# Kernel tuning notes

Measured on AMD Instinct MI355X. Metric: run time of the kernel, lower is better.

The kernel has to match this reference:

```python
import jax, jax.numpy as jnp
import numpy as np

C, H, W, D, M = 64, 512, 512, 4, 16


def setup_inputs() -> dict:
    key = jax.random.key(0)
    ks = jax.random.split(key, 9)
    scale = (1.0 / (C * C)) ** 0.5
    return {
        "q": jax.random.normal(ks[0], (1, 1, H, W), jnp.float32),
        "proj_w": jax.random.normal(ks[1], (C, 1, 1, 1), jnp.float32),
        "proj_b": jax.random.normal(ks[2], (C, 1, 1), jnp.float32) * 0.01,
        "spec_wr": jax.random.normal(ks[3], (D, C, C, M, M), jnp.float32) * scale,
        "spec_wi": jax.random.normal(ks[4], (D, C, C, M, M), jnp.float32) * scale,
        "w_w": jax.random.normal(ks[5], (D, C, C, 1, 1), jnp.float32) * (1.0 / C ** 0.5),
        "w_b": jax.random.normal(ks[6], (D, C, 1, 1), jnp.float32) * 0.01,
        "final_w": jax.random.normal(ks[7], (1, C, 1, 1), jnp.float32) * (1.0 / C ** 0.5),
        "final_b": jax.random.normal(ks[8], (1, 1, 1), jnp.float32) * 0.01,
    }


def _spectral(x, wr, wi, m):
    # x: (C,H,W). FFT2 -> contract low modes -> zero-pad -> iFFT2, take real part.
    Cin, Hh, Ww = x.shape
    x_ft = jnp.fft.fft2(x, axes=(-2, -1))  # (C,H,W) complex
    w = (wr + 1j * wi).astype(x_ft.dtype)  # (Cin,Cout,m,m)
    out_sub = jnp.einsum('imn,iomn->omn', x_ft[:, :m, :m], w)
    out_ft = jnp.zeros((wr.shape[1], Hh, Ww), dtype=x_ft.dtype).at[:, :m, :m].set(out_sub)
    return jnp.fft.ifft2(out_ft, axes=(-2, -1)).real


def reference(q, proj_w, proj_b, spec_wr, spec_wi, w_w, w_b, final_w, final_b):
    m = spec_wr.shape[-1]
    depth = spec_wr.shape[0]
    x = q[0].astype(jnp.float32)  # (C_in,H,W) -- batch must be 1
    # 1x1 conv lift
    x = jnp.einsum('oi,ihw->ohw', proj_w[:, :, 0, 0], x) + proj_b
    for d in range(depth):
        x_spec = _spectral(x, spec_wr[d], spec_wi[d], m)
        x_local = jnp.einsum('oi,ihw->ohw', w_w[d, :, :, 0, 0], x) + w_b[d]
        x = jax.nn.gelu(x_spec + x_local)
    x = jnp.einsum('oi,ihw->ohw', final_w[:, :, 0, 0], x) + final_b
    return x[None]  # re-add batch dim
```

## Files before the change

kernel.cpp:

```cpp
#include <hip/hip_runtime.h>
#include <cmath>

#define CC 64
#define HH 512
#define WWID 512
#define HWSZ (HH*WWID)
#define DEPTH 4

typedef __attribute__((ext_vector_type(8))) short short8;
typedef __attribute__((ext_vector_type(4))) float floatx4;

__device__ inline unsigned short f2bf(float f){
  unsigned int u = __float_as_uint(f);
  u += 0x7FFF + ((u >> 16) & 1);
  return (unsigned short)(u >> 16);
}
__device__ inline float bf2f(unsigned short h){
  return __uint_as_float(((unsigned int)h) << 16);
}

__global__ void k_init(const float* __restrict__ ww,
                       float* __restrict__ ctab, float* __restrict__ stab,
                       unsigned short* __restrict__ trigBh, unsigned short* __restrict__ trigBl,
                       unsigned short* __restrict__ trigTh, unsigned short* __restrict__ trigTl,
                       unsigned short* __restrict__ Whi, unsigned short* __restrict__ Wlo,
                       float4* __restrict__ Xfz){
  if (blockIdx.x < 32) Xfz[blockIdx.x*256 + threadIdx.x] = make_float4(0.f,0.f,0.f,0.f);
  int idx = blockIdx.x*256 + threadIdx.x;
  if (idx < 8192){
    int pos = idx >> 4, k = idx & 15;
    int r = (pos * k) & 511;
    double ang = (2.0 * 3.14159265358979323846 / 512.0) * (double)r;
    float c = (float)cos(ang), s = (float)sin(ang);
    ctab[idx] = c;  stab[idx] = s;
    unsigned short ch = f2bf(c), sh = f2bf(s);
    unsigned short cl = f2bf(c - bf2f(ch)), sl = f2bf(s - bf2f(sh));
    trigBh[pos*32 + 2*k]     = ch;  trigBl[pos*32 + 2*k]     = cl;
    trigBh[pos*32 + 2*k + 1] = sh;  trigBl[pos*32 + 2*k + 1] = sl;
    trigTh[(2*k)*512 + pos]   = ch;  trigTl[(2*k)*512 + pos]   = cl;
    trigTh[(2*k+1)*512 + pos] = sh;  trigTl[(2*k+1)*512 + pos] = sl;
  } else {
    int t = idx - 8192;
    float v = ww[t];
    unsigned short h = f2bf(v);
    Whi[t] = h;  Wlo[t] = f2bf(v - bf2f(h));
  }
}

#define APITCH 136
#define XPITCH 33
template<int LIFT>
__global__ __launch_bounds__(256) void k_dftw(const unsigned int* __restrict__ xp,
    const float* __restrict__ qsrc, const float* __restrict__ pw, const float* __restrict__ pb,
    const unsigned short* __restrict__ trigTh, const unsigned short* __restrict__ trigTl,
    const float* __restrict__ ctab, const float* __restrict__ stab,
    float* __restrict__ Xfa, float4* __restrict__ Yz){
  if (blockIdx.x < 32) Yz[blockIdx.x*256 + threadIdx.x] = make_float4(0.f,0.f,0.f,0.f);

  __shared__ unsigned short Ahs[64*APITCH], Als[64*APITCH];
  __shared__ unsigned short Bhs[32*APITCH], Bls[32*APITCH];
  __shared__ float X1s[64*XPITCH];
  int row0 = blockIdx.x * 64;
  int i  = row0 >> 9;
  int h0 = row0 & 511;
  int t = threadIdx.x;
  int g = t >> 6, lm = t & 15, lq = (t >> 4) & 3;
  float pa = 0.f, pbv = 0.f;
  if (LIFT){ pa = pw[i]; pbv = pb[i]; }

  floatx4 acc[2] = {{0.f,0.f,0.f,0.f},{0.f,0.f,0.f,0.f}};

  for (int kc = 0; kc < 4; ++kc){
    {
      int r = t >> 2, qq = t & 3;
      unsigned int* dh = (unsigned int*)&Ahs[r*APITCH + qq*32];
      unsigned int* dl = (unsigned int*)&Als[r*APITCH + qq*32];
      if (LIFT){
        const float4* src4 = (const float4*)(qsrc + (size_t)(h0 + r)*512 + kc*128 + qq*32);
        #pragma unroll
        for (int u = 0; u < 8; ++u){
          float4 v = src4[u];
          v.x = fmaf(pa, v.x, pbv); v.y = fmaf(pa, v.y, pbv);
          v.z = fmaf(pa, v.z, pbv); v.w = fmaf(pa, v.w, pbv);
          unsigned short h0_ = f2bf(v.x), h1 = f2bf(v.y), h2 = f2bf(v.z), h3 = f2bf(v.w);
          unsigned short g0 = f2bf(v.x - bf2f(h0_)), g1 = f2bf(v.y - bf2f(h1));
          unsigned short g2 = f2bf(v.z - bf2f(h2)), g3 = f2bf(v.w - bf2f(h3));
          uint2 ph, pl;
          ph.x = (unsigned)h0_ | ((unsigned)h1 << 16);
          ph.y = (unsigned)h2 | ((unsigned)h3 << 16);
          pl.x = (unsigned)g0 | ((unsigned)g1 << 16);
          pl.y = (unsigned)g2 | ((unsigned)g3 << 16);
          *(uint2*)&dh[u*2] = ph;
          *(uint2*)&dl[u*2] = pl;
        }
      } else {
        const uint4* srcp = (const uint4*)(xp + ((size_t)(h0 + r)*64 + i)*512 + kc*128 + qq*32);
        #pragma unroll
        for (int u = 0; u < 8; ++u){
          uint4 v = srcp[u];
          uint2 ph, pl;
          ph.x = (v.x & 0xffffu) | (v.y << 16);
          ph.y = (v.z & 0xffffu) | (v.w << 16);
          pl.x = (v.x >> 16) | (v.y & 0xffff0000u);
          pl.y = (v.z >> 16) | (v.w & 0xffff0000u);
          *(uint2*)&dh[u*2] = ph;
          *(uint2*)&dl[u*2] = pl;
        }
      }
    }
    {
      int j = t >> 3, qq = t & 7;
      const uint4* sh = (const uint4*)((const unsigned int*)trigTh + j*256 + kc*64 + qq*8);
      const uint4* sl = (const uint4*)((const unsigned int*)trigTl + j*256 + kc*64 + qq*8);
      uint4* dh = (uint4*)&Bhs[j*APITCH + qq*16];
      uint4* dl = (uint4*)&Bls[j*APITCH + qq*16];
      dh[0] = sh[0]; dh[1] = sh[1];
      dl[0] = sl[0]; dl[1] = sl[1];
    }
    __syncthreads();
    #pragma unroll
    for (int ks = 0; ks < 4; ++ks){
      short8 ah = *(const short8*)&Ahs[(g*16 + lm)*APITCH + ks*32 + lq*8];
      short8 al = *(const short8*)&Als[(g*16 + lm)*APITCH + ks*32 + lq*8];
      #pragma unroll
      for (int nt = 0; nt < 2; ++nt){
        short8 bh = *(const short8*)&Bhs[(nt*16 + lm)*APITCH + ks*32 + lq*8];
        short8 bl = *(const short8*)&Bls[(nt*16 + lm)*APITCH + ks*32 + lq*8];
        acc[nt] = __builtin_amdgcn_mfma_f32_16x16x32_bf16(ah, bh, acc[nt], 0, 0, 0);
        acc[nt] = __builtin_amdgcn_mfma_f32_16x16x32_bf16(ah, bl, acc[nt], 0, 0, 0);
        acc[nt] = __builtin_amdgcn_mfma_f32_16x16x32_bf16(al, bh, acc[nt], 0, 0, 0);
      }
    }
    __syncthreads();
  }
  #pragma unroll
  for (int nt = 0; nt < 2; ++nt){
    int j = nt*16 + lm;
    float sgn = (j & 1) ? -1.f : 1.f;
    #pragma unroll
    for (int rg = 0; rg < 4; ++rg){
      int m = g*16 + lq*4 + rg;
      X1s[m*XPITCH + j] = sgn * acc[nt][rg];
    }
  }
  __syncthreads();

  int mo = t >> 4, n = t & 15;
  float ar = 0.f, ai = 0.f;
  #pragma unroll 8
  for (int hh = 0; hh < 64; ++hh){
    int h = h0 + hh;
    float Re = X1s[hh*XPITCH + 2*n];
    float Im = X1s[hh*XPITCH + 2*n + 1];
    float c = ctab[h*16 + mo], s = stab[h*16 + mo];
    ar += Re*c + Im*s;
    ai += Im*c - Re*s;
  }
  atomicAdd(&Xfa[(i*256 + t)*2],     ar);
  atomicAdd(&Xfa[(i*256 + t)*2 + 1], ai);
}

__global__ void k_contract(const float2* __restrict__ Xf,
                           const float* __restrict__ wr, const float* __restrict__ wi,
                           float* __restrict__ Ya){
  int o = blockIdx.x, ic = blockIdx.y;
  int mn = blockIdx.z*64 + threadIdx.x;
  float ar = 0.f, ai = 0.f;
  int i0 = ic * 16;
  #pragma unroll
  for (int ii = 0; ii < 16; ++ii){
    int i = i0 + ii;
    float2 xf = Xf[i*256 + mn];
    float wrv = wr[(i*64 + o)*256 + mn];
    float wiv = wi[(i*64 + o)*256 + mn];
    ar += xf.x*wrv - xf.y*wiv;
    ai += xf.x*wiv + xf.y*wrv;
  }
  const float sc = 1.f/262144.f;
  atomicAdd(&Ya[(o*256 + mn)*2],     ar*sc);
  atomicAdd(&Ya[(o*256 + mn)*2 + 1], ai*sc);
}

__global__ void k_idfth(const float2* __restrict__ Y, const float* __restrict__ ct,
                        const float* __restrict__ st,
                        unsigned int* __restrict__ Thi, unsigned int* __restrict__ Tlo,
                        float4* __restrict__ Xfz){
  if (blockIdx.x < 32) Xfz[blockIdx.x*256 + threadIdx.x] = make_float4(0.f,0.f,0.f,0.f);
  int idx = blockIdx.x*256 + threadIdx.x;
  int n = idx & 15, o = (idx >> 4) & 63, h = idx >> 10;
  float ar = 0.f, ai = 0.f;
  #pragma unroll
  for (int m = 0; m < 16; ++m){
    float2 y = Y[(o<<8) + (m<<4) + n];
    float c = ct[h*16 + m], s = st[h*16 + m];
    ar += y.x*c - y.y*s;
    ai += y.x*s + y.y*c;
  }
  float tr = ar, ts = -ai;
  unsigned short rh = f2bf(tr), sh = f2bf(ts);
  Thi[idx] = (unsigned int)rh | ((unsigned int)sh << 16);
  unsigned short rl = f2bf(tr - bf2f(rh)), slr = f2bf(ts - bf2f(sh));
  Tlo[idx] = (unsigned int)rl | ((unsigned int)slr << 16);
}

#define PITCH 104
template<int LIFT, int FINAL>
__global__ __launch_bounds__(256) void k_combine(
    const unsigned int* __restrict__ xp, const float* __restrict__ qsrc,
    const float* __restrict__ pw, const float* __restrict__ pb,
    const unsigned short* __restrict__ Whid, const unsigned short* __restrict__ Wlod,
    const unsigned int* __restrict__ Thi,  const unsigned int* __restrict__ Tlo,
    const unsigned short* __restrict__ trigBh, const unsigned short* __restrict__ trigBl,
    const float* __restrict__ wb, unsigned int* __restrict__ xo,
    const float* __restrict__ fw, const float* __restrict__ fb,
    float* __restrict__ outp)
{
  __shared__ unsigned short Ah[64*PITCH], Al[64*PITCH];
  int h  = blockIdx.y;
  int w0 = blockIdx.x * 128;
  int t  = threadIdx.x;

  {
    int o = t >> 2, q8 = t & 3;
    const uint4* sh = (const uint4*)((const unsigned int*)Whid + o*32 + q8*8);
    const uint4* sl = (const uint4*)((const unsigned int*)Wlod + o*32 + q8*8);
    uint4* dh = (uint4*)((unsigned int*)&Ah[o*PITCH] + q8*8);
    uint4* dl = (uint4*)((unsigned int*)&Al[o*PITCH] + q8*8);
    dh[0] = sh[0]; dh[1] = sh[1];
    dl[0] = sl[0]; dl[1] = sl[1];
  }
  {
    int o = t >> 2, q4 = t & 3;
    const uint4* sh = (const uint4*)(Thi + (size_t)h*1024 + o*16 + q4*4);
    const uint4* sl = (const uint4*)(Tlo + (size_t)h*1024 + o*16 + q4*4);
    uint4* dh = (uint4*)((unsigned int*)&Ah[o*PITCH + 64] + q4*4);
    uint4* dl = (uint4*)((unsigned int*)&Al[o*PITCH + 64] + q4*4);
    dh[0] = sh[0];
    dl[0] = sl[0];
  }
  __syncthreads();

  int g  = t >> 6;
  int lm = t & 15;
  int lq = (t >> 4) & 3;
  int wbase = w0 + g*32;

  const unsigned int* xw = xp + (size_t)h*32768;
  float pwv[16], pbv[16];
  if (LIFT){
    #pragma unroll
    for (int u = 0; u < 8; ++u){
      pwv[u]   = pw[lq*8 + u];      pbv[u]   = pb[lq*8 + u];
      pwv[8+u] = pw[32 + lq*8 + u]; pbv[8+u] = pb[32 + lq*8 + u];
    }
  }

  short8 bf0[2], bl0[2], bf1[2], bl1[2], bf2[2], bl2[2];
  #pragma unroll
  for (int nt = 0; nt < 2; ++nt){
    int w = wbase + nt*16 + lm;
    unsigned int v0[8], v1[8];
    if (LIFT){
      float qv = qsrc[(size_t)h*512 + w];
      #pragma unroll
      for (int u = 0; u < 8; ++u){
        float a = fmaf(pwv[u], qv, pbv[u]);
        unsigned short hh = f2bf(a), ll = f2bf(a - bf2f(hh));
        v0[u] = (unsigned int)hh | ((unsigned int)ll << 16);
        float b = fmaf(pwv[8+u], qv, pbv[8+u]);
        unsigned short hb = f2bf(b), lb = f2bf(b - bf2f(hb));
        v1[u] = (unsigned int)hb | ((unsigned int)lb << 16);
      }
    } else {
      #pragma unroll
      for (int u = 0; u < 8; ++u){
        v0[u] = xw[(size_t)(     lq*8 + u)*512 + w];
        v1[u] = xw[(size_t)(32 + lq*8 + u)*512 + w];
      }
    }
    unsigned int f0[4], l0[4], f1[4], l1[4];
    #pragma unroll
    for (int p = 0; p < 4; ++p){
      f0[p] = (v0[2*p] & 0xffffu) | (v0[2*p+1] << 16);
      l0[p] = (v0[2*p] >> 16)     | (v0[2*p+1] & 0xffff0000u);
      f1[p] = (v1[2*p] & 0xffffu) | (v1[2*p+1] << 16);
      l1[p] = (v1[2*p] >> 16)     | (v1[2*p+1] & 0xffff0000u);
    }
    bf0[nt] = *(short8*)f0;  bl0[nt] = *(short8*)l0;
    bf1[nt] = *(short8*)f1;  bl1[nt] = *(short8*)l1;
    bf2[nt] = *(const short8*)(trigBh + (size_t)w*32 + lq*8);
    bl2[nt] = *(const short8*)(trigBl + (size_t)w*32 + lq*8);
  }

  floatx4 acc[8] = {{0.f,0.f,0.f,0.f},{0.f,0.f,0.f,0.f},{0.f,0.f,0.f,0.f},{0.f,0.f,0.f,0.f},
                    {0.f,0.f,0.f,0.f},{0.f,0.f,0.f,0.f},{0.f,0.f,0.f,0.f},{0.f,0.f,0.f,0.f}};

  #pragma unroll
  for (int m = 0; m < 4; ++m){
    short8 af0 = *(const short8*)&Ah[(m*16 + lm)*PITCH +  0 + lq*8];
    short8 al0 = *(const short8*)&Al[(m*16 + lm)*PITCH +  0 + lq*8];
    short8 af1 = *(const short8*)&Ah[(m*16 + lm)*PITCH + 32 + lq*8];
    short8 al1 = *(const short8*)&Al[(m*16 + lm)*PITCH + 32 + lq*8];
    short8 af2 = *(const short8*)&Ah[(m*16 + lm)*PITCH + 64 + lq*8];
    short8 al2 = *(const short8*)&Al[(m*16 + lm)*PITCH + 64 + lq*8];
    #pragma unroll
    for (int nt = 0; nt < 2; ++nt){
      int a = m*2 + nt;
      acc[a] = __builtin_amdgcn_mfma_f32_16x16x32_bf16(af0, bf0[nt], acc[a], 0, 0, 0);
      acc[a] = __builtin_amdgcn_mfma_f32_16x16x32_bf16(af0, bl0[nt], acc[a], 0, 0, 0);
      acc[a] = __builtin_amdgcn_mfma_f32_16x16x32_bf16(al0, bf0[nt], acc[a], 0, 0, 0);
      acc[a] = __builtin_amdgcn_mfma_f32_16x16x32_bf16(af1, bf1[nt], acc[a], 0, 0, 0);
      acc[a] = __builtin_amdgcn_mfma_f32_16x16x32_bf16(af1, bl1[nt], acc[a], 0, 0, 0);
      acc[a] = __builtin_amdgcn_mfma_f32_16x16x32_bf16(al1, bf1[nt], acc[a], 0, 0, 0);
      acc[a] = __builtin_amdgcn_mfma_f32_16x16x32_bf16(af2, bf2[nt], acc[a], 0, 0, 0);
      acc[a] = __builtin_amdgcn_mfma_f32_16x16x32_bf16(af2, bl2[nt], acc[a], 0, 0, 0);
      acc[a] = __builtin_amdgcn_mfma_f32_16x16x32_bf16(al2, bf2[nt], acc[a], 0, 0, 0);
    }
  }

  if (!FINAL){
    #pragma unroll
    for (int m = 0; m < 4; ++m){
      #pragma unroll
      for (int nt = 0; nt < 2; ++nt){
        int w = wbase + nt*16 + lm;
        #pragma unroll
        for (int rg = 0; rg < 4; ++rg){
          int o = m*16 + lq*4 + rg;
          float u = acc[m*2+nt][rg] + wb[o];
          float z = 0.7978845608028654f * fmaf(0.044715f, u*u*u, u);
          float e = __expf(2.f*z);
          float gl = u - __fdividef(u, e + 1.f);
          unsigned short hi_ = f2bf(gl);
          unsigned short lo_ = f2bf(gl - bf2f(hi_));
          xo[((size_t)h*64 + o)*512 + w] = (unsigned int)hi_ | ((unsigned int)lo_ << 16);
        }
      }
    }
  } else {
    float* fred = (float*)Ah;
    __syncthreads();
    #pragma unroll
    for (int nt = 0; nt < 2; ++nt){
      float partial = 0.f;
      #pragma unroll
      for (int m = 0; m < 4; ++m){
        #pragma unroll
        for (int rg = 0; rg < 4; ++rg){
          int o = m*16 + lq*4 + rg;
          float u = acc[m*2+nt][rg] + wb[o];
          float z = 0.7978845608028654f * fmaf(0.044715f, u*u*u, u);
          float e = __expf(2.f*z);
          float gl = u - __fdividef(u, e + 1.f);
          partial = fmaf(fw[o], gl, partial);
        }
      }
      int wl = g*32 + nt*16 + lm;
      fred[wl*17 + lq] = partial;
    }
    __syncthreads();
    if (t < 128){
      float s = fb[0];
      #pragma unroll
      for (int k2 = 0; k2 < 4; ++k2) s += fred[t*17 + k2];
      outp[(size_t)h*512 + w0 + t] = s;
    }
  }
}

extern "C" void kernel_launch(void* const* d_in, const int* in_sizes, int n_in,
                              void* d_out, int out_size, void* d_ws, size_t ws_size,
                              hipStream_t stream) {
  const float* q       = (const float*)d_in[0];
  const float* proj_w  = (const float*)d_in[1];
  const float* proj_b  = (const float*)d_in[2];
  const float* spec_wr = (const float*)d_in[3];
  const float* spec_wi = (const float*)d_in[4];
  const float* w_w     = (const float*)d_in[5];
  const float* w_b     = (const float*)d_in[6];
  const float* final_w = (const float*)d_in[7];
  const float* final_b = (const float*)d_in[8];
  float* out = (float*)d_out;

  char* ws = (char*)d_ws;
  float*  ctab = (float*) (ws + 0);
  float*  stab = (float*) (ws + 32768);
  unsigned short* trigBh = (unsigned short*)(ws + 65536);
  unsigned short* trigBl = (unsigned short*)(ws + 98304);
  unsigned int* Thi = (unsigned int*)(ws + 131072);
  unsigned int* Tlo = (unsigned int*)(ws + 2228224);
  float*  Xf   = (float*) (ws + 4325376);
  float*  Y    = (float*) (ws + 4456448);
  unsigned int* x = (unsigned int*)(ws + 4587520);
  unsigned short* Whi = (unsigned short*)(ws + 71696384);
  unsigned short* Wlo = (unsigned short*)(ws + 71729152);
  unsigned short* trigTh = (unsigned short*)(ws + 71761920);
  unsigned short* trigTl = (unsigned short*)(ws + 71794688);

  k_init<<<96, 256, 0, stream>>>(w_w, ctab, stab, trigBh, trigBl, trigTh, trigTl,
                                 Whi, Wlo, (float4*)Xf);

  for (int d = 0; d < DEPTH; ++d){
    if (d == 0)
      k_dftw<1><<<512, 256, 0, stream>>>(x, q, proj_w, proj_b, trigTh, trigTl,
                                         ctab, stab, Xf, (float4*)Y);
    else
      k_dftw<0><<<512, 256, 0, stream>>>(x, q, proj_w, proj_b, trigTh, trigTl,
                                         ctab, stab, Xf, (float4*)Y);
    k_contract<<<dim3(64,4,4), 64, 0, stream>>>((const float2*)Xf,
                                                spec_wr + (size_t)d*1048576,
                                                spec_wi + (size_t)d*1048576, Y);
    k_idfth<<<2048, 256, 0, stream>>>((const float2*)Y, ctab, stab, Thi, Tlo,
                                      (float4*)Xf);
    if (d == 0)
      k_combine<1,0><<<dim3(4,512), 256, 0, stream>>>(x, q, proj_w, proj_b,
          Whi + d*4096, Wlo + d*4096, Thi, Tlo, trigBh, trigBl,
          w_b + d*64, x, final_w, final_b, out);
    else if (d < DEPTH-1)
      k_combine<0,0><<<dim3(4,512), 256, 0, stream>>>(x, q, proj_w, proj_b,
          Whi + d*4096, Wlo + d*4096, Thi, Tlo, trigBh, trigBl,
          w_b + d*64, x, final_w, final_b, out);
    else
      k_combine<0,1><<<dim3(4,512), 256, 0, stream>>>(x, q, proj_w, proj_b,
          Whi + d*4096, Wlo + d*4096, Thi, Tlo, trigBh, trigBl,
          w_b + d*64, x, final_w, final_b, out);
  }
}
```

Baseline: 327.9 us.

## Load DFT MFMA operands directly from global memory, dropping LDS staging

The W-direction DFT kernel no longer stages the activation rows and trig tables through shared memory with syncthreads per K chunk. Each lane now loads its MFMA A and B fragments straight from global memory (or q with the lift applied) and does the bf16 hi/lo split in registers. This removes the LDS round trip, the barriers and the shared-memory footprint, which may raise occupancy. In exchange, trig fragments are read redundantly per wave through the cache, and the global loads are less coalesced.

```diff
diff --git a/kernel.cpp b/kernel.cpp
--- a/kernel.cpp
+++ b/kernel.cpp
@@ -47,7 +47,6 @@
   }
 }
 
-#define APITCH 136
 #define XPITCH 33
 template<int LIFT>
 __global__ __launch_bounds__(256) void k_dftw(const unsigned int* __restrict__ xp,
@@ -57,8 +56,6 @@
     float* __restrict__ Xfa, float4* __restrict__ Yz){
   if (blockIdx.x < 32) Yz[blockIdx.x*256 + threadIdx.x] = make_float4(0.f,0.f,0.f,0.f);
 
-  __shared__ unsigned short Ahs[64*APITCH], Als[64*APITCH];
-  __shared__ unsigned short Bhs[32*APITCH], Bls[32*APITCH];
   __shared__ float X1s[64*XPITCH];
   int row0 = blockIdx.x * 64;
   int i  = row0 >> 9;
@@ -70,69 +67,52 @@
 
   floatx4 acc[2] = {{0.f,0.f,0.f,0.f},{0.f,0.f,0.f,0.f}};
 
-  for (int kc = 0; kc < 4; ++kc){
-    {
-      int r = t >> 2, qq = t & 3;
-      unsigned int* dh = (unsigned int*)&Ahs[r*APITCH + qq*32];
-      unsigned int* dl = (unsigned int*)&Als[r*APITCH + qq*32];
-      if (LIFT){
-        const float4* src4 = (const float4*)(qsrc + (size_t)(h0 + r)*512 + kc*128 + qq*32);
-        #pragma unroll
-        for (int u = 0; u < 8; ++u){
-          float4 v = src4[u];
-          v.x = fmaf(pa, v.x, pbv); v.y = fmaf(pa, v.y, pbv);
-          v.z = fmaf(pa, v.z, pbv); v.w = fmaf(pa, v.w, pbv);
-          unsigned short h0_ = f2bf(v.x), h1 = f2bf(v.y), h2 = f2bf(v.z), h3 = f2bf(v.w);
-          unsigned short g0 = f2bf(v.x - bf2f(h0_)), g1 = f2bf(v.y - bf2f(h1));
-          unsigned short g2 = f2bf(v.z - bf2f(h2)), g3 = f2bf(v.w - bf2f(h3));
-          uint2 ph, pl;
-          ph.x = (unsigned)h0_ | ((unsigned)h1 << 16);
-          ph.y = (unsigned)h2 | ((unsigned)h3 << 16);
-          pl.x = (unsigned)g0 | ((unsigned)g1 << 16);
-          pl.y = (unsigned)g2 | ((unsigned)g3 << 16);
-          *(uint2*)&dh[u*2] = ph;
-          *(uint2*)&dl[u*2] = pl;
-        }
-      } else {
-        const uint4* srcp = (const uint4*)(xp + ((size_t)(h0 + r)*64 + i)*512 + kc*128 + qq*32);
-        #pragma unroll
-        for (int u = 0; u < 8; ++u){
-          uint4 v = srcp[u];
-          uint2 ph, pl;
-          ph.x = (v.x & 0xffffu) | (v.y << 16);
-          ph.y = (v.z & 0xffffu) | (v.w << 16);
-          pl.x = (v.x >> 16) | (v.y & 0xffff0000u);
-          pl.y = (v.z >> 16) | (v.w & 0xffff0000u);
-          *(uint2*)&dh[u*2] = ph;
-          *(uint2*)&dl[u*2] = pl;
-        }
-      }
-    }
-    {
-      int j = t >> 3, qq = t & 7;
-      const uint4* sh = (const uint4*)((const unsigned int*)trigTh + j*256 + kc*64 + qq*8);
-      const uint4* sl = (const uint4*)((const unsigned int*)trigTl + j*256 + kc*64 + qq*8);
-      uint4* dh = (uint4*)&Bhs[j*APITCH + qq*16];
-      uint4* dl = (uint4*)&Bls[j*APITCH + qq*16];
-      dh[0] = sh[0]; dh[1] = sh[1];
-      dl[0] = sl[0]; dl[1] = sl[1];
-    }
-    __syncthreads();
-    #pragma unroll
-    for (int ks = 0; ks < 4; ++ks){
-      short8 ah = *(const short8*)&Ahs[(g*16 + lm)*APITCH + ks*32 + lq*8];
-      short8 al = *(const short8*)&Als[(g*16 + lm)*APITCH + ks*32 + lq*8];
-      #pragma unroll
-      for (int nt = 0; nt < 2; ++nt){
-        short8 bh = *(const short8*)&Bhs[(nt*16 + lm)*APITCH + ks*32 + lq*8];
-        short8 bl = *(const short8*)&Bls[(nt*16 + lm)*APITCH + ks*32 + lq*8];
-        acc[nt] = __builtin_amdgcn_mfma_f32_16x16x32_bf16(ah, bh, acc[nt], 0, 0, 0);
-        acc[nt] = __builtin_amdgcn_mfma_f32_16x16x32_bf16(ah, bl, acc[nt], 0, 0, 0);
-        acc[nt] = __builtin_amdgcn_mfma_f32_16x16x32_bf16(al, bh, acc[nt], 0, 0, 0);
-      }
-    }
-    __syncthreads();
-  }
+  int hrow = h0 + g*16 + lm;
+  const unsigned int* arow = xp + ((size_t)hrow*64 + i)*512;
+  const float*        qrow = qsrc + (size_t)hrow*512;
+
+  #pragma unroll 4
+  for (int ch = 0; ch < 16; ++ch){
+    int kb = ch*32 + lq*8;
+    short8 ah, al;
+    if (LIFT){
+      float4 qa = *(const float4*)(qrow + kb);
+      float4 qb = *(const float4*)(qrow + kb + 4);
+      float v[8] = {qa.x,qa.y,qa.z,qa.w,qb.x,qb.y,qb.z,qb.w};
+      unsigned int hs[4], ls[4];
+      #pragma unroll
+      for (int p = 0; p < 4; ++p){
+        float v0 = fmaf(pa, v[2*p],   pbv);
+        float v1 = fmaf(pa, v[2*p+1], pbv);
+        unsigned short hh0 = f2bf(v0), hh1 = f2bf(v1);
+        unsigned short gg0 = f2bf(v0 - bf2f(hh0)), gg1 = f2bf(v1 - bf2f(hh1));
+        hs[p] = (unsigned)hh0 | ((unsigned)hh1 << 16);
+        ls[p] = (unsigned)gg0 | ((unsigned)gg1 << 16);
+      }
+      ah = *(short8*)hs;  al = *(short8*)ls;
+    } else {
+      uint4 va = *(const uint4*)(arow + kb);
+      uint4 vb = *(const uint4*)(arow + kb + 4);
+      unsigned int u[8] = {va.x,va.y,va.z,va.w,vb.x,vb.y,vb.z,vb.w};
+      unsigned int hs[4], ls[4];
+      #pragma unroll
+      for (int p = 0; p < 4; ++p){
+        hs[p] = (u[2*p] & 0xffffu) | (u[2*p+1] << 16);
+        ls[p] = (u[2*p] >> 16)     | (u[2*p+1] & 0xffff0000u);
+      }
+      ah = *(short8*)hs;  al = *(short8*)ls;
+    }
+    #pragma unroll
+    for (int nt = 0; nt < 2; ++nt){
+      int j = nt*16 + lm;
+      short8 bh = *(const short8*)(trigTh + (size_t)j*512 + kb);
+      short8 bl = *(const short8*)(trigTl + (size_t)j*512 + kb);
+      acc[nt] = __builtin_amdgcn_mfma_f32_16x16x32_bf16(ah, bh, acc[nt], 0, 0, 0);
+      acc[nt] = __builtin_amdgcn_mfma_f32_16x16x32_bf16(ah, bl, acc[nt], 0, 0, 0);
+      acc[nt] = __builtin_amdgcn_mfma_f32_16x16x32_bf16(al, bh, acc[nt], 0, 0, 0);
+    }
+  }
+
   #pragma unroll
   for (int nt = 0; nt < 2; ++nt){
     int j = nt*16 + lm;
```

Result: slower. 398.6 us (+21.6%).
